# Kernel optimization log

Measured on AMD Instinct MI355X. Metric: run time of the kernel, lower is better.

Reference implementation:

```python
import jax, jax.numpy as jnp
import numpy as np

GAMMA = 0.99   # discount_factor
LAM = 0.95     # smoothing_factor

def setup_inputs() -> dict:
    key = jax.random.key(0)
    k1, k2, k3, k4 = jax.random.split(key, 4)
    B, T = 4096, 2048
    return {
        "rewards": jax.random.normal(k1, (B, T), dtype=jnp.float32),
        "values": jax.random.normal(k2, (B, T), dtype=jnp.float32),
        "next_value": jax.random.normal(k3, (B,), dtype=jnp.float32),
        "done_flags": jax.random.randint(k4, (B, T), 0, 2, dtype=jnp.int32),
    }

def reference(rewards, values, next_value, done_flags):
    d = done_flags.astype(rewards.dtype)
    # next_non_terminal[t] = 1 - done[t+1] for t < T-1, and 1 - done[T-1] at t = T-1
    nnt = 1.0 - jnp.concatenate([d[..., 1:], d[..., -1:]], axis=-1)
    # next value at step t: values[t+1] for t < T-1, bootstrap next_value at t = T-1
    nv = jnp.concatenate([values[..., 1:], next_value[..., None]], axis=-1)
    delta = rewards + GAMMA * nv * nnt - values  # [B, T]

    def step(gae, x):
        dl, nn = x
        gae = dl + GAMMA * LAM * nn * gae
        return gae, gae

    # scan backward over time (leading axis for lax.scan)
    deltaT = jnp.moveaxis(delta, -1, 0)  # [T, B]
    nntT = jnp.moveaxis(nnt, -1, 0)      # [T, B]
    init = jnp.zeros(rewards.shape[:-1], rewards.dtype)
    _, advT = jax.lax.scan(step, init, (deltaT, nntT), reverse=True)
    advantages = jnp.moveaxis(advT, 0, -1)  # [B, T]
    returns = advantages + values
    return advantages, returns
```

## Files before the change

kernel.cpp:

```cpp
#include <hip/hip_runtime.h>

#define GAMMA 0.99f
#define LAM   0.95f

constexpr int CHUNK = 32;
constexpr int WPB   = 4;
constexpr int BLOCK = WPB * 64;

__global__ __launch_bounds__(BLOCK) void gae_wave_kernel(
    const float* __restrict__ rewards,
    const float* __restrict__ values,
    const float* __restrict__ next_value,
    const int*   __restrict__ done,
    float* __restrict__ adv_out,
    float* __restrict__ ret_out,
    int B, int T)
{
    const int wave = threadIdx.x >> 6;
    const int lane = threadIdx.x & 63;
    const int row  = blockIdx.x * WPB + wave;
    if (row >= B) return;

    const long rowbase = (long)row * T;
    const int  col0    = lane * CHUNK;

    const float4* r4 = reinterpret_cast<const float4*>(rewards + rowbase + col0);
    const float4* v4 = reinterpret_cast<const float4*>(values  + rowbase + col0);
    const int4*   d4 = reinterpret_cast<const int4*>(done      + rowbase + col0);

    float4 ra[8], va[8];
    int4   da[8];
#pragma unroll
    for (int k = 0; k < 8; ++k) { ra[k] = r4[k]; }
#pragma unroll
    for (int k = 0; k < 8; ++k) { va[k] = v4[k]; }
#pragma unroll
    for (int k = 0; k < 8; ++k) { da[k] = d4[k]; }
    const float vboot = next_value[row];

    float v[CHUNK], r[CHUNK];
    int   d[CHUNK];
#pragma unroll
    for (int k = 0; k < 8; ++k) {
        v[4*k+0]=va[k].x; v[4*k+1]=va[k].y; v[4*k+2]=va[k].z; v[4*k+3]=va[k].w;
        r[4*k+0]=ra[k].x; r[4*k+1]=ra[k].y; r[4*k+2]=ra[k].z; r[4*k+3]=ra[k].w;
        d[4*k+0]=da[k].x; d[4*k+1]=da[k].y; d[4*k+2]=da[k].z; d[4*k+3]=da[k].w;
    }

    const float v_nb = __shfl_down(v[0], 1);
    const int   d_nb = __shfl_down(d[0], 1);
    const float vnext  = (lane == 63) ? vboot : v_nb;
    const int   dnext  = (lane == 63) ? d[CHUNK-1] : d_nb;

    float delta[CHUNK], c[CHUNK];
#pragma unroll
    for (int j = 0; j < CHUNK; ++j) {
        const int   dn  = (j < CHUNK-1) ? d[j+1] : dnext;
        const float nv  = (j < CHUNK-1) ? v[j+1] : vnext;
        const float nnt = 1.0f - (float)dn;
        delta[j] = r[j] + GAMMA * nv * nnt - v[j];
        c[j]     = (GAMMA * LAM) * nnt;
    }

    float a = 0.0f, m = 1.0f;
#pragma unroll
    for (int j = CHUNK - 1; j >= 0; --j) {
        a = delta[j] + c[j] * a;
        m = c[j] * m;
    }

    float sa = a, sm = m;
#pragma unroll
    for (int dd = 1; dd < 64; dd <<= 1) {
        float oa = __shfl_down(sa, dd);
        float om = __shfl_down(sm, dd);
        if (lane + dd < 64) { sa = sa + sm * oa; sm = sm * om; }
    }
    float gin = __shfl_down(sa, 1);
    if (lane == 63) gin = 0.0f;

#pragma unroll
    for (int j = CHUNK - 1; j >= 0; --j) {
        gin = delta[j] + c[j] * gin;
        delta[j] = gin;
    }

    float4* a4 = reinterpret_cast<float4*>(adv_out + rowbase + col0);
    float4* t4 = reinterpret_cast<float4*>(ret_out + rowbase + col0);
#pragma unroll
    for (int k = 0; k < 8; ++k)
        a4[k] = make_float4(delta[4*k+0], delta[4*k+1], delta[4*k+2], delta[4*k+3]);
#pragma unroll
    for (int k = 0; k < 8; ++k)
        t4[k] = make_float4(delta[4*k+0]+v[4*k+0], delta[4*k+1]+v[4*k+1],
                            delta[4*k+2]+v[4*k+2], delta[4*k+3]+v[4*k+3]);
}

__global__ void gae_naive_kernel(
    const float* __restrict__ rewards,
    const float* __restrict__ values,
    const float* __restrict__ next_value,
    const int*   __restrict__ done,
    float* __restrict__ adv_out,
    float* __restrict__ ret_out,
    int B, int T)
{
    int row = blockIdx.x * blockDim.x + threadIdx.x;
    if (row >= B) return;
    long base = (long)row * T;
    float g = 0.0f;
    for (int t = T - 1; t >= 0; --t) {
        int dcol = (t + 1 < T) ? (t + 1) : (T - 1);
        float nnt = 1.0f - (float)done[base + dcol];
        float nv  = (t + 1 < T) ? values[base + t + 1] : next_value[row];
        float dl  = rewards[base + t] + GAMMA * nv * nnt - values[base + t];
        g = dl + (GAMMA * LAM) * nnt * g;
        adv_out[base + t] = g;
        ret_out[base + t] = g + values[base + t];
    }
}

extern "C" void kernel_launch(void* const* d_in, const int* in_sizes, int n_in,
                              void* d_out, int out_size, void* d_ws, size_t ws_size,
                              hipStream_t stream) {
    const float* rewards    = (const float*)d_in[0];
    const float* values     = (const float*)d_in[1];
    const float* next_value = (const float*)d_in[2];
    const int*   done       = (const int*)d_in[3];

    const int B = in_sizes[2];
    const int T = in_sizes[0] / B;

    float* adv = (float*)d_out;
    float* ret = adv + (long)B * T;

    if (T == 64 * CHUNK) {
        const int grid = (B + WPB - 1) / WPB;
        gae_wave_kernel<<<grid, BLOCK, 0, stream>>>(
            rewards, values, next_value, done, adv, ret, B, T);
    } else {
        gae_naive_kernel<<<(B + 255) / 256, 256, 0, stream>>>(
            rewards, values, next_value, done, adv, ret, B, T);
    }
}
```

Before: 158.1 us.

## Process GAE rows in coalesced 256-column passes with a carried scan

```diff
diff --git a/kernel.cpp b/kernel.cpp
--- a/kernel.cpp
+++ b/kernel.cpp
@@ -3,9 +3,9 @@
 #define GAMMA 0.99f
 #define LAM   0.95f
 
-constexpr int CHUNK = 32;
-constexpr int WPB   = 4;
-constexpr int BLOCK = WPB * 64;
+constexpr int WPB       = 4;
+constexpr int BLOCK     = WPB * 64;
+constexpr int PASS_COLS = 256;
 
 __global__ __launch_bounds__(BLOCK) void gae_wave_kernel(
     const float* __restrict__ rewards,
@@ -22,78 +22,92 @@
     if (row >= B) return;
 
     const long rowbase = (long)row * T;
-    const int  col0    = lane * CHUNK;
+    const int  npass   = T / PASS_COLS;
 
-    const float4* r4 = reinterpret_cast<const float4*>(rewards + rowbase + col0);
-    const float4* v4 = reinterpret_cast<const float4*>(values  + rowbase + col0);
-    const int4*   d4 = reinterpret_cast<const int4*>(done      + rowbase + col0);
+    const float4* r4 = reinterpret_cast<const float4*>(rewards + rowbase);
+    const float4* v4 = reinterpret_cast<const float4*>(values  + rowbase);
+    const int4*   d4 = reinterpret_cast<const int4*>(done      + rowbase);
+    float4* a4 = reinterpret_cast<float4*>(adv_out + rowbase);
+    float4* t4 = reinterpret_cast<float4*>(ret_out + rowbase);
 
-    float4 ra[8], va[8];
-    int4   da[8];
-#pragma unroll
-    for (int k = 0; k < 8; ++k) { ra[k] = r4[k]; }
-#pragma unroll
-    for (int k = 0; k < 8; ++k) { va[k] = v4[k]; }
-#pragma unroll
-    for (int k = 0; k < 8; ++k) { da[k] = d4[k]; }
     const float vboot = next_value[row];
 
-    float v[CHUNK], r[CHUNK];
-    int   d[CHUNK];
+    auto LD = [&](int p, float4& R, float4& V, int4& D) {
+        const int idx = p * 64 + lane;
+        R = r4[idx]; V = v4[idx]; D = d4[idx];
+    };
+
+    float4 cr, cv, nr, nv2;
+    int4   cd, nd;
+    LD(npass - 1, cr, cv, cd);
+
+    float pv_bc = 0.0f;
+    float pd_bc = 0.0f;
+    float g     = 0.0f;
+
+    for (int p = npass - 1; p >= 0; --p) {
+        if (p > 0) LD(p - 1, nr, nv2, nd);
+
+        const bool last = (p == npass - 1);
+
+        const float v_nb = __shfl_down(cv.x, 1);
+        const int   d_nb = __shfl_down(cd.x, 1);
+        float vnext  = (lane == 63) ? (last ? vboot : pv_bc) : v_nb;
+        float dnextf = (lane == 63) ? (last ? (float)cd.w : pd_bc) : (float)d_nb;
+
+        const float dn0 = (float)cd.y, dn1 = (float)cd.z, dn2 = (float)cd.w;
+        float delta[4], c[4];
+        {
+            const float nnt0 = 1.0f - dn0;
+            const float nnt1 = 1.0f - dn1;
+            const float nnt2 = 1.0f - dn2;
+            const float nnt3 = 1.0f - dnextf;
+            delta[0] = cr.x + GAMMA * cv.y  * nnt0 - cv.x;
+            delta[1] = cr.y + GAMMA * cv.z  * nnt1 - cv.y;
+            delta[2] = cr.z + GAMMA * cv.w  * nnt2 - cv.z;
+            delta[3] = cr.w + GAMMA * vnext * nnt3 - cv.w;
+            c[0] = (GAMMA * LAM) * nnt0;
+            c[1] = (GAMMA * LAM) * nnt1;
+            c[2] = (GAMMA * LAM) * nnt2;
+            c[3] = (GAMMA * LAM) * nnt3;
+        }
+
+        float a = 0.0f, m = 1.0f;
 #pragma unroll
-    for (int k = 0; k < 8; ++k) {
-        v[4*k+0]=va[k].x; v[4*k+1]=va[k].y; v[4*k+2]=va[k].z; v[4*k+3]=va[k].w;
-        r[4*k+0]=ra[k].x; r[4*k+1]=ra[k].y; r[4*k+2]=ra[k].z; r[4*k+3]=ra[k].w;
-        d[4*k+0]=da[k].x; d[4*k+1]=da[k].y; d[4*k+2]=da[k].z; d[4*k+3]=da[k].w;
+        for (int j = 3; j >= 0; --j) {
+            a = delta[j] + c[j] * a;
+            m = c[j] * m;
+        }
+
+        float sa = a, sm = m;
+#pragma unroll
+        for (int dd = 1; dd < 64; dd <<= 1) {
+            float oa = __shfl_down(sa, dd);
+            float om = __shfl_down(sm, dd);
+            if (lane + dd < 64) { sa = sa + sm * oa; sm = sm * om; }
+        }
+        float ea = __shfl_down(sa, 1);
+        float em = __shfl_down(sm, 1);
+        if (lane == 63) { ea = 0.0f; em = 1.0f; }
+
+        float gin = ea + em * g;
+#pragma unroll
+        for (int j = 3; j >= 0; --j) {
+            gin = delta[j] + c[j] * gin;
+            delta[j] = gin;
+        }
+
+        const int idx = p * 64 + lane;
+        a4[idx] = make_float4(delta[0], delta[1], delta[2], delta[3]);
+        t4[idx] = make_float4(delta[0] + cv.x, delta[1] + cv.y,
+                              delta[2] + cv.z, delta[3] + cv.w);
+
+        pv_bc = __shfl(cv.x, 0);
+        pd_bc = (float)__shfl(cd.x, 0);
+        g     = __shfl(sa, 0) + __shfl(sm, 0) * g;
+
+        cr = nr; cv = nv2; cd = nd;
     }
-
-    const float v_nb = __shfl_down(v[0], 1);
-    const int   d_nb = __shfl_down(d[0], 1);
-    const float vnext  = (lane == 63) ? vboot : v_nb;
-    const int   dnext  = (lane == 63) ? d[CHUNK-1] : d_nb;
-
-    float delta[CHUNK], c[CHUNK];
-#pragma unroll
-    for (int j = 0; j < CHUNK; ++j) {
-        const int   dn  = (j < CHUNK-1) ? d[j+1] : dnext;
-        const float nv  = (j < CHUNK-1) ? v[j+1] : vnext;
-        const float nnt = 1.0f - (float)dn;
-        delta[j] = r[j] + GAMMA * nv * nnt - v[j];
-        c[j]     = (GAMMA * LAM) * nnt;
-    }
-
-    float a = 0.0f, m = 1.0f;
-#pragma unroll
-    for (int j = CHUNK - 1; j >= 0; --j) {
-        a = delta[j] + c[j] * a;
-        m = c[j] * m;
-    }
-
-    float sa = a, sm = m;
-#pragma unroll
-    for (int dd = 1; dd < 64; dd <<= 1) {
-        float oa = __shfl_down(sa, dd);
-        float om = __shfl_down(sm, dd);
-        if (lane + dd < 64) { sa = sa + sm * oa; sm = sm * om; }
-    }
-    float gin = __shfl_down(sa, 1);
-    if (lane == 63) gin = 0.0f;
-
-#pragma unroll
-    for (int j = CHUNK - 1; j >= 0; --j) {
-        gin = delta[j] + c[j] * gin;
-        delta[j] = gin;
-    }
-
-    float4* a4 = reinterpret_cast<float4*>(adv_out + rowbase + col0);
-    float4* t4 = reinterpret_cast<float4*>(ret_out + rowbase + col0);
-#pragma unroll
-    for (int k = 0; k < 8; ++k)
-        a4[k] = make_float4(delta[4*k+0], delta[4*k+1], delta[4*k+2], delta[4*k+3]);
-#pragma unroll
-    for (int k = 0; k < 8; ++k)
-        t4[k] = make_float4(delta[4*k+0]+v[4*k+0], delta[4*k+1]+v[4*k+1],
-                            delta[4*k+2]+v[4*k+2], delta[4*k+3]+v[4*k+3]);
 }
 
 __global__ void gae_naive_kernel(
@@ -134,7 +148,7 @@
     float* adv = (float*)d_out;
     float* ret = adv + (long)B * T;
 
-    if (T == 64 * CHUNK) {
+    if (T % PASS_COLS == 0 && T >= PASS_COLS) {
         const int grid = (B + WPB - 1) / WPB;
         gae_wave_kernel<<<grid, BLOCK, 0, stream>>>(
             rewards, values, next_value, done, adv, ret, B, T);
```

Measured after the change: 151.0 us. -4.5%, faster.
